# Kernel optimization log

Measured on AMD Instinct MI355X. Metric: run time of the kernel, lower is better.

Reference implementation:

```python
import jax, jax.numpy as jnp
import numpy as np

DIM = 1024
EXP = 4           # expansion_factor
NUM_EXPERTS = 4
BATCH, SEQ = 4, 4096


def setup_inputs() -> dict:
    key = jax.random.key(0)
    ks = jax.random.split(key, 6)
    x = jax.random.normal(ks[0], (BATCH, SEQ, DIM), dtype=jnp.float32)
    token_mask = jax.random.randint(ks[1], (BATCH, SEQ), 0, NUM_EXPERTS, dtype=jnp.int32)
    hid = DIM * EXP
    s1 = 1.0 / np.sqrt(DIM)
    s2 = 1.0 / np.sqrt(hid)
    # nn.Linear layout: weight [out_features, in_features]
    w1 = jax.random.uniform(ks[2], (hid, DIM), minval=-s1, maxval=s1, dtype=jnp.float32)
    b1 = jax.random.uniform(ks[3], (hid,), minval=-s1, maxval=s1, dtype=jnp.float32)
    w2 = jax.random.uniform(ks[4], (DIM, hid), minval=-s2, maxval=s2, dtype=jnp.float32)
    b2 = jax.random.uniform(ks[5], (DIM,), minval=-s2, maxval=s2, dtype=jnp.float32)
    return {"x": x, "w1": w1, "b1": b1, "w2": w2, "b2": b2, "token_mask": token_mask}


def _nested_ffn(x, w1, b1, w2, b2, token_mask):
    dim = x.shape[-1]            # in_features of proj1
    out_dim = w2.shape[0]        # out_features of proj2 (== dim)
    # Expert m uses the first D_m = width >> (E-1-m) features (matryoshka nesting).
    # Expand (proj1): truncating input features to D_m and doing a full GEMM is
    # exactly equivalent to zeroing features >= D_m, so we mask then do one GEMM.
    d_in = dim >> (NUM_EXPERTS - 1 - token_mask)             # [B,S]
    in_mask = jnp.arange(dim) < d_in[..., None]              # [B,S,dim]
    h = jnp.einsum('bsd,fd->bsf', jnp.where(in_mask, x, jnp.zeros((), x.dtype)), w1) + b1
    h = jax.nn.gelu(h, approximate=False)                    # torch nn.GELU() default = erf
    # Contract (proj2): expert m produces only the first D_m outputs (incl. bias),
    # padded with zeros -> compute full GEMM then mask outputs.
    d_out = out_dim >> (NUM_EXPERTS - 1 - token_mask)        # [B,S]
    out_mask = jnp.arange(out_dim) < d_out[..., None]        # [B,S,out_dim]
    y = jnp.einsum('bsf,df->bsd', h, w2) + b2
    return jnp.where(out_mask, y, jnp.zeros((), y.dtype))


def reference(x, w1, b1, w2, b2, token_mask):
    return _nested_ffn(x, w1, b1, w2, b2, token_mask)
```

## Files before the change

kernel.cpp:

```cpp
#include <hip/hip_runtime.h>
#include <hip/hip_bf16.h>


typedef __bf16 bf16x8 __attribute__((ext_vector_type(8)));
typedef float f32x4 __attribute__((ext_vector_type(4)));

#define M_TOK   16384
#define DIM     1024
#define HID     4096

#define META_TK    40
#define META_BLK   64
#define META_MAP   256
#define META_RT    2560

__device__ inline unsigned int pk_bf16(float a, float b) {
  unsigned int r;
  asm("v_cvt_pk_bf16_f32 %0, %1, %2" : "=v"(r) : "v"(a), "v"(b));
  return r;
}

__device__ inline float gelu_f(float v) {
  float v2 = v * v;
  float w = v * fmaf(0.10294324f, v2, 2.30220830f);
  float e = __builtin_amdgcn_exp2f(-w);
  return v * __builtin_amdgcn_rcpf(1.0f + e);
}

__device__ inline void async_copy16(const void* g, void* s) {
  __builtin_amdgcn_global_load_lds(
      (const __attribute__((address_space(1))) unsigned int*)g,
      (__attribute__((address_space(3))) unsigned int*)s,
      16, 0, 0);
}

template<int ROWS, int LDK>
__device__ inline void stage_tile(const unsigned short* __restrict__ g,
                                  int row0, int k0, char* lds) {
  const char* gbase = (const char*)g;
  int tid = threadIdx.x;
#pragma unroll
  for (int i = 0; i < ROWS / 32; ++i) {
    int q = i * 256 + tid;
    int r = q >> 3;
    int c = q & 7;
    int gc = c ^ (r & 7);
    const void* gp = gbase + ((size_t)(row0 + r) * LDK + (size_t)k0 + gc * 8) * 2;
    async_copy16(gp, lds + (size_t)q * 16);
  }
}

__global__ __launch_bounds__(1024) void sortw_kernel(
    const int* __restrict__ tm,
    const float* __restrict__ w1,
    const float* __restrict__ w2,
    int* __restrict__ meta,
    unsigned short* __restrict__ w1b,
    unsigned short* __restrict__ w2b) {
  int tid = threadIdx.x;
  if (blockIdx.x != 0) {
    size_t i = (size_t)(blockIdx.x - 1) * 4096 + tid * 4;
    const float* src;
    unsigned short* dst;
    if (i < (size_t)HID * DIM) { src = w1; dst = w1b; }
    else { src = w2 - (size_t)HID * DIM; dst = w2b - (size_t)HID * DIM; }
    float4 v = *(const float4*)(src + i);
    uint2 o;
    o.x = pk_bf16(v.x, v.y);
    o.y = pk_bf16(v.z, v.w);
    *(uint2*)(dst + i) = o;
    return;
  }

  __shared__ unsigned short rt[16384];
  __shared__ unsigned int w01[16], w23[16];
  __shared__ int sbase[4];
  __shared__ int cb[128];
  int lane = tid & 63, wv = tid >> 6;

  int c0 = 0, c1 = 0, c2 = 0, c3 = 0;
  unsigned int epack = 0;
  int4 tv[4];
#pragma unroll
  for (int j = 0; j < 4; ++j)
    tv[j] = *(const int4*)(tm + tid * 16 + j * 4);
#pragma unroll
  for (int j = 0; j < 4; ++j) {
    int e;
    e = tv[j].x; epack |= (unsigned)e << (2 * (4 * j + 0)); c0 += (e == 0); c1 += (e == 1); c2 += (e == 2); c3 += (e == 3);
    e = tv[j].y; epack |= (unsigned)e << (2 * (4 * j + 1)); c0 += (e == 0); c1 += (e == 1); c2 += (e == 2); c3 += (e == 3);
    e = tv[j].z; epack |= (unsigned)e << (2 * (4 * j + 2)); c0 += (e == 0); c1 += (e == 1); c2 += (e == 2); c3 += (e == 3);
    e = tv[j].w; epack |= (unsigned)e << (2 * (4 * j + 3)); c0 += (e == 0); c1 += (e == 1); c2 += (e == 2); c3 += (e == 3);
  }
  unsigned int p01 = (unsigned)c0 | ((unsigned)c1 << 16);
  unsigned int p23 = (unsigned)c2 | ((unsigned)c3 << 16);
  unsigned int i01 = p01, i23 = p23;
#pragma unroll
  for (int s = 1; s < 64; s <<= 1) {
    unsigned int t0 = __shfl_up(i01, s, 64);
    unsigned int t1 = __shfl_up(i23, s, 64);
    if (lane >= s) { i01 += t0; i23 += t1; }
  }
  if (lane == 63) { w01[wv] = i01; w23[wv] = i23; }
  unsigned int e01 = i01 - p01, e23 = i23 - p23;
  __syncthreads();
  if (tid < 16) {
    unsigned int a = w01[tid], b = w23[tid];
    unsigned int ia = a, ib = b;
#pragma unroll
    for (int s = 1; s < 16; s <<= 1) {
      unsigned int t0 = __shfl_up(ia, s, 64);
      unsigned int t1 = __shfl_up(ib, s, 64);
      if (tid >= s) { ia += t0; ib += t1; }
    }
    w01[tid] = ia - a;
    w23[tid] = ib - b;
    if (tid == 15) {
      int t0 = (int)(ia & 0xFFFF), t1 = (int)(ia >> 16), t2 = (int)(ib & 0xFFFF);
      sbase[0] = 0; sbase[1] = t0; sbase[2] = t0 + t1; sbase[3] = t0 + t1 + t2;
    }
  }
  __syncthreads();
  int off0 = sbase[0] + (int)((w01[wv] & 0xFFFF) + (e01 & 0xFFFF));
  int off1 = sbase[1] + (int)((w01[wv] >> 16) + (e01 >> 16));
  int off2 = sbase[2] + (int)((w23[wv] & 0xFFFF) + (e23 & 0xFFFF));
  int off3 = sbase[3] + (int)((w23[wv] >> 16) + (e23 >> 16));
#pragma unroll
  for (int j = 0; j < 16; ++j) {
    int e = (epack >> (2 * j)) & 3;
    int t = tid * 16 + j;
    int pos = (e == 0) ? off0++ : (e == 1) ? off1++ : (e == 2) ? off2++ : off3++;
    rt[pos] = (unsigned short)(t | (e << 14));
  }
  __syncthreads();

  if (tid < 128) {
    int last = tid * 128 + 127;
    int e = (last >= sbase[1]) + (last >= sbase[2]) + (last >= sbase[3]);
    cb[tid] = 1 << e;
    meta[META_BLK + tid] = 128 << e;
  }
  __syncthreads();
  if (tid < 8) {
    int k = tid;
    int* map = meta + META_MAP + k * 128;
    int Tk = 0;
    for (int j = 0; j < 16; ++j) Tk += cb[k + 8 * j];
    meta[META_TK + k] = Tk;
    int pos = 0, zpos = Tk;
    for (int j = 0; j < 16; ++j) {
      int s = k + 8 * j;
      int n = cb[s];
      for (int c = 0; c < n; ++c) map[pos++] = s * 8 + c;
      for (int c = n; c < 8; ++c) map[zpos++] = s * 8 + c;
    }
  }
  int* rowtok = meta + META_RT;
#pragma unroll
  for (int j = 0; j < 16; ++j)
    rowtok[j * 1024 + tid] = (int)rt[j * 1024 + tid];
}

__global__ void prepx_kernel(const float* __restrict__ x,
                             const int* __restrict__ meta,
                             unsigned short* __restrict__ xb) {
  int b = blockIdx.x;
  int tid = threadIdx.x;
  int mt = meta[META_RT + b];
  int t = mt & 0x3FFF;
  int din = 128 << (mt >> 14);
  int kb = meta[META_BLK + (b >> 7)];
  int d = tid * 4;
  if (d < kb) {
    uint2 o; o.x = 0; o.y = 0;
    if (d < din) {
      float4 v = *(const float4*)(x + (size_t)t * DIM + d);
      o.x = pk_bf16(v.x, v.y);
      o.y = pk_bf16(v.z, v.w);
    }
    *(uint2*)(xb + (size_t)b * DIM + d) = o;
  }
}

__global__ __launch_bounds__(256) void gemm1_kernel(
    const unsigned short* __restrict__ A,
    const unsigned short* __restrict__ B,
    const float* __restrict__ bias,
    const int* __restrict__ meta,
    unsigned short* __restrict__ H)
{
  constexpr int K = DIM, N = HID;
  __shared__ char smem[65536];
  int tid = threadIdx.x;
  int lane = tid & 63, quad = lane >> 4, l15 = lane & 15;
  int wave = tid >> 6, wm = wave & 1, wn = wave >> 1;
  int rowblk = 127 - (blockIdx.x >> 5);
  int row0 = rowblk * 128, col0 = (blockIdx.x & 31) * 128;
  int kmax = meta[META_BLK + rowblk];

  int chb = (quad ^ (l15 & 7)) << 4;

  f32x4 acc[4][4] = {};

  stage_tile<128, K>(A, row0, 0, smem);
  stage_tile<128, K>(B, col0, 0, smem + 16384);

  int nt = kmax >> 6;
  for (int t = 0; t < nt; ++t) {
    char* buf = smem + ((t & 1) << 15);
    if (t + 1 < nt) {
      char* nbuf = smem + (((t + 1) & 1) << 15);
      int kn = (t + 1) << 6;
      stage_tile<128, K>(A, row0, kn, nbuf);
      stage_tile<128, K>(B, col0, kn, nbuf + 16384);
      asm volatile("s_waitcnt vmcnt(8)" ::: "memory");
    } else {
      asm volatile("s_waitcnt vmcnt(0)" ::: "memory");
    }
    __builtin_amdgcn_s_barrier();
    char* As = buf;
    char* Bs = buf + 16384;
#pragma unroll
    for (int kk = 0; kk < 2; ++kk) {
      int xo = chb ^ (kk << 6);
      bf16x8 af[4], bg[4];
#pragma unroll
      for (int mt = 0; mt < 4; ++mt)
        af[mt] = *(const bf16x8*)(As + (wm * 64 + mt * 16 + l15) * 128 + xo);
#pragma unroll
      for (int nt2 = 0; nt2 < 4; ++nt2)
        bg[nt2] = *(const bf16x8*)(Bs + (wn * 64 + nt2 * 16 + l15) * 128 + xo);
#pragma unroll
      for (int mt = 0; mt < 4; ++mt)
#pragma unroll
        for (int nt2 = 0; nt2 < 4; ++nt2)
          acc[mt][nt2] = __builtin_amdgcn_mfma_f32_16x16x32_bf16(
              bg[nt2], af[mt], acc[mt][nt2], 0, 0, 0);
    }
    __builtin_amdgcn_s_barrier();
  }

  int t_base = row0 + wm * 64;
  int f_base = col0 + wn * 64;
#pragma unroll
  for (int nt2 = 0; nt2 < 4; ++nt2) {
    int f0 = f_base + nt2 * 16 + quad * 4;
    float4 bv = *(const float4*)(bias + f0);
#pragma unroll
    for (int mt = 0; mt < 4; ++mt) {
      int t = t_base + mt * 16 + l15;
      float v0 = gelu_f(acc[mt][nt2][0] + bv.x);
      float v1 = gelu_f(acc[mt][nt2][1] + bv.y);
      float v2 = gelu_f(acc[mt][nt2][2] + bv.z);
      float v3 = gelu_f(acc[mt][nt2][3] + bv.w);
      uint2 p;
      p.x = pk_bf16(v0, v1);
      p.y = pk_bf16(v2, v3);
      *(uint2*)(H + (size_t)t * N + f0) = p;
    }
  }
}

__global__ __launch_bounds__(256) void gemm2_kernel(
    const unsigned short* __restrict__ A,
    const unsigned short* __restrict__ B,
    const float* __restrict__ bias,
    const int* __restrict__ meta,
    float* __restrict__ out)
{
  constexpr int K = HID, N = DIM;
  int Bk = blockIdx.x & 7, ord = blockIdx.x >> 3;
  int Tk = meta[META_TK + Bk];
  int mp = meta[META_MAP + Bk * 128 + ord];
  int row0 = (mp >> 3) * 128, col0 = (mp & 7) * 128;
  const int* rowtok = meta + META_RT;
  int tid = threadIdx.x;

  if (ord >= Tk) {
    float4 z = make_float4(0.f, 0.f, 0.f, 0.f);
#pragma unroll
    for (int i = 0; i < 16; ++i) {
      int idx = i * 256 + tid;
      int r = idx >> 5;
      int col = (idx & 31) * 4;
      int t = rowtok[row0 + r] & 0x3FFF;
      *(float4*)(out + (size_t)t * N + col0 + col) = z;
    }
    return;
  }

  __shared__ char smem[65536];
  int lane = tid & 63, quad = lane >> 4, l15 = lane & 15;
  int wave = tid >> 6, wm = wave & 1, wn = wave >> 1;
  int chb = (quad ^ (l15 & 7)) << 4;

  f32x4 acc[4][4] = {};

  stage_tile<128, K>(A, row0, 0, smem);
  stage_tile<128, K>(B, col0, 0, smem + 16384);

  constexpr int NT = K >> 6;
  for (int t = 0; t < NT; ++t) {
    char* buf = smem + ((t & 1) << 15);
    if (t + 1 < NT) {
      char* nbuf = smem + (((t + 1) & 1) << 15);
      int kn = (t + 1) << 6;
      stage_tile<128, K>(A, row0, kn, nbuf);
      stage_tile<128, K>(B, col0, kn, nbuf + 16384);
      asm volatile("s_waitcnt vmcnt(8)" ::: "memory");
    } else {
      asm volatile("s_waitcnt vmcnt(0)" ::: "memory");
    }
    __builtin_amdgcn_s_barrier();
    char* As = buf;
    char* Bs = buf + 16384;
#pragma unroll
    for (int kk = 0; kk < 2; ++kk) {
      int xo = chb ^ (kk << 6);
      bf16x8 af[4], bg[4];
#pragma unroll
      for (int mt = 0; mt < 4; ++mt)
        af[mt] = *(const bf16x8*)(As + (wm * 64 + mt * 16 + l15) * 128 + xo);
#pragma unroll
      for (int nt2 = 0; nt2 < 4; ++nt2)
        bg[nt2] = *(const bf16x8*)(Bs + (wn * 64 + nt2 * 16 + l15) * 128 + xo);
#pragma unroll
      for (int mt = 0; mt < 4; ++mt)
#pragma unroll
        for (int nt2 = 0; nt2 < 4; ++nt2)
          acc[mt][nt2] = __builtin_amdgcn_mfma_f32_16x16x32_bf16(
              bg[nt2], af[mt], acc[mt][nt2], 0, 0, 0);
    }
    __builtin_amdgcn_s_barrier();
  }

  int p_base = row0 + wm * 64;
  int d_base = col0 + wn * 64;
  float4 bv[4];
#pragma unroll
  for (int nt2 = 0; nt2 < 4; ++nt2)
    bv[nt2] = *(const float4*)(bias + d_base + nt2 * 16 + quad * 4);
#pragma unroll
  for (int mt = 0; mt < 4; ++mt) {
    int m2 = rowtok[p_base + mt * 16 + l15];
    int t = m2 & 0x3FFF;
    int dout = 128 << (m2 >> 14);
#pragma unroll
    for (int nt2 = 0; nt2 < 4; ++nt2) {
      int d0 = d_base + nt2 * 16 + quad * 4;
      bool ok = d0 < dout;
      float4 o;
      o.x = ok ? acc[mt][nt2][0] + bv[nt2].x : 0.0f;
      o.y = ok ? acc[mt][nt2][1] + bv[nt2].y : 0.0f;
      o.z = ok ? acc[mt][nt2][2] + bv[nt2].z : 0.0f;
      o.w = ok ? acc[mt][nt2][3] + bv[nt2].w : 0.0f;
      *(float4*)(out + (size_t)t * N + d0) = o;
    }
  }
}

extern "C" void kernel_launch(void* const* d_in, const int* in_sizes, int n_in,
                              void* d_out, int out_size, void* d_ws, size_t ws_size,
                              hipStream_t stream) {
  const float* x  = (const float*)d_in[0];
  const float* w1 = (const float*)d_in[1];
  const float* b1 = (const float*)d_in[2];
  const float* w2 = (const float*)d_in[3];
  const float* b2 = (const float*)d_in[4];
  const int*   tm = (const int*)d_in[5];
  float* out = (float*)d_out;

  char* ws = (char*)d_ws;
  int* meta = (int*)ws;
  unsigned short* xb  = (unsigned short*)(ws + 131072);
  unsigned short* w1b = (unsigned short*)(ws + 33685504);
  unsigned short* w2b = (unsigned short*)(ws + 42074112);
  unsigned short* hb  = (unsigned short*)(ws + 50462720);

  sortw_kernel<<<2049, 1024, 0, stream>>>(tm, w1, w2, meta, w1b, w2b);
  prepx_kernel<<<M_TOK, 256, 0, stream>>>(x, meta, xb);
  gemm1_kernel<<<4096, 256, 0, stream>>>(xb, w1b, b1, meta, hb);
  gemm2_kernel<<<1024, 256, 0, stream>>>(hb, w2b, b2, meta, out);
}
```

Before: 302.6 us.

## Widen gemm2 tiles to 128x256 with 512-thread blocks and setprio

Changes gemm2 from 128x128 tiles with 256 threads to 128x256 tiles with 8 waves and 512 threads. It rebuilds the per-expert column-block map in the sort kernel for 4 column blocks per row block. It also raises wave priority around the MFMA section. The goal is to reuse each A tile across twice as many output columns, halving A traffic from the hidden buffer. The cost is 96KB of LDS per block, which limits occupancy, and coarser granularity for the masked column blocks.

Result: slower. 365.3 us (+20.7%).

```diff
diff --git a/kernel.cpp b/kernel.cpp
--- a/kernel.cpp
+++ b/kernel.cpp
@@ -34,14 +34,14 @@
       16, 0, 0);
 }
 
-template<int ROWS, int LDK>
+template<int ROWS, int LDK, int THREADS>
 __device__ inline void stage_tile(const unsigned short* __restrict__ g,
                                   int row0, int k0, char* lds) {
   const char* gbase = (const char*)g;
   int tid = threadIdx.x;
 #pragma unroll
-  for (int i = 0; i < ROWS / 32; ++i) {
-    int q = i * 256 + tid;
+  for (int i = 0; i < ROWS * 8 / THREADS; ++i) {
+    int q = i * THREADS + tid;
     int r = q >> 3;
     int c = q & 7;
     int gc = c ^ (r & 7);
@@ -137,13 +137,13 @@
   if (tid < 128) {
     int last = tid * 128 + 127;
     int e = (last >= sbase[1]) + (last >= sbase[2]) + (last >= sbase[3]);
-    cb[tid] = 1 << e;
     meta[META_BLK + tid] = 128 << e;
+    cb[tid] = (e < 2) ? 1 : (1 << (e - 1));
   }
   __syncthreads();
   if (tid < 8) {
     int k = tid;
-    int* map = meta + META_MAP + k * 128;
+    int* map = meta + META_MAP + k * 64;
     int Tk = 0;
     for (int j = 0; j < 16; ++j) Tk += cb[k + 8 * j];
     meta[META_TK + k] = Tk;
@@ -151,8 +151,8 @@
     for (int j = 0; j < 16; ++j) {
       int s = k + 8 * j;
       int n = cb[s];
-      for (int c = 0; c < n; ++c) map[pos++] = s * 8 + c;
-      for (int c = n; c < 8; ++c) map[zpos++] = s * 8 + c;
+      for (int c = 0; c < n; ++c) map[pos++] = s * 4 + c;
+      for (int c = n; c < 4; ++c) map[zpos++] = s * 4 + c;
     }
   }
   int* rowtok = meta + META_RT;
@@ -202,8 +202,8 @@
 
   f32x4 acc[4][4] = {};
 
-  stage_tile<128, K>(A, row0, 0, smem);
-  stage_tile<128, K>(B, col0, 0, smem + 16384);
+  stage_tile<128, K, 256>(A, row0, 0, smem);
+  stage_tile<128, K, 256>(B, col0, 0, smem + 16384);
 
   int nt = kmax >> 6;
   for (int t = 0; t < nt; ++t) {
@@ -211,8 +211,8 @@
     if (t + 1 < nt) {
       char* nbuf = smem + (((t + 1) & 1) << 15);
       int kn = (t + 1) << 6;
-      stage_tile<128, K>(A, row0, kn, nbuf);
-      stage_tile<128, K>(B, col0, kn, nbuf + 16384);
+      stage_tile<128, K, 256>(A, row0, kn, nbuf);
+      stage_tile<128, K, 256>(B, col0, kn, nbuf + 16384);
       asm volatile("s_waitcnt vmcnt(8)" ::: "memory");
     } else {
       asm volatile("s_waitcnt vmcnt(0)" ::: "memory");
@@ -261,7 +261,7 @@
   }
 }
 
-__global__ __launch_bounds__(256) void gemm2_kernel(
+__global__ __launch_bounds__(512, 2) void gemm2_kernel(
     const unsigned short* __restrict__ A,
     const unsigned short* __restrict__ B,
     const float* __restrict__ bias,
@@ -271,8 +271,8 @@
   constexpr int K = HID, N = DIM;
   int Bk = blockIdx.x & 7, ord = blockIdx.x >> 3;
   int Tk = meta[META_TK + Bk];
-  int mp = meta[META_MAP + Bk * 128 + ord];
-  int row0 = (mp >> 3) * 128, col0 = (mp & 7) * 128;
+  int mp = meta[META_MAP + Bk * 64 + ord];
+  int row0 = (mp >> 2) * 128, col0 = (mp & 3) * 256;
   const int* rowtok = meta + META_RT;
   int tid = threadIdx.x;
 
@@ -280,40 +280,42 @@
     float4 z = make_float4(0.f, 0.f, 0.f, 0.f);
 #pragma unroll
     for (int i = 0; i < 16; ++i) {
-      int idx = i * 256 + tid;
-      int r = idx >> 5;
-      int col = (idx & 31) * 4;
+      int idx = i * 512 + tid;
+      int r = idx >> 6;
+      int col = (idx & 63) * 4;
       int t = rowtok[row0 + r] & 0x3FFF;
       *(float4*)(out + (size_t)t * N + col0 + col) = z;
     }
     return;
   }
 
-  __shared__ char smem[65536];
+  __shared__ char smem[98304];
   int lane = tid & 63, quad = lane >> 4, l15 = lane & 15;
-  int wave = tid >> 6, wm = wave & 1, wn = wave >> 1;
+  int wave = tid >> 6;
+  int wm = wave >> 2, wn = wave & 3;
   int chb = (quad ^ (l15 & 7)) << 4;
 
   f32x4 acc[4][4] = {};
 
-  stage_tile<128, K>(A, row0, 0, smem);
-  stage_tile<128, K>(B, col0, 0, smem + 16384);
+  stage_tile<128, K, 512>(A, row0, 0, smem);
+  stage_tile<256, K, 512>(B, col0, 0, smem + 16384);
 
   constexpr int NT = K >> 6;
   for (int t = 0; t < NT; ++t) {
-    char* buf = smem + ((t & 1) << 15);
+    char* buf = smem + (t & 1) * 49152;
     if (t + 1 < NT) {
-      char* nbuf = smem + (((t + 1) & 1) << 15);
+      char* nbuf = smem + ((t + 1) & 1) * 49152;
       int kn = (t + 1) << 6;
-      stage_tile<128, K>(A, row0, kn, nbuf);
-      stage_tile<128, K>(B, col0, kn, nbuf + 16384);
-      asm volatile("s_waitcnt vmcnt(8)" ::: "memory");
+      stage_tile<128, K, 512>(A, row0, kn, nbuf);
+      stage_tile<256, K, 512>(B, col0, kn, nbuf + 16384);
+      asm volatile("s_waitcnt vmcnt(6)" ::: "memory");
     } else {
       asm volatile("s_waitcnt vmcnt(0)" ::: "memory");
     }
     __builtin_amdgcn_s_barrier();
     char* As = buf;
     char* Bs = buf + 16384;
+    __builtin_amdgcn_s_setprio(1);
 #pragma unroll
     for (int kk = 0; kk < 2; ++kk) {
       int xo = chb ^ (kk << 6);
@@ -322,15 +324,16 @@
       for (int mt = 0; mt < 4; ++mt)
         af[mt] = *(const bf16x8*)(As + (wm * 64 + mt * 16 + l15) * 128 + xo);
 #pragma unroll
-      for (int nt2 = 0; nt2 < 4; ++nt2)
-        bg[nt2] = *(const bf16x8*)(Bs + (wn * 64 + nt2 * 16 + l15) * 128 + xo);
+      for (int nf = 0; nf < 4; ++nf)
+        bg[nf] = *(const bf16x8*)(Bs + (wn * 64 + nf * 16 + l15) * 128 + xo);
 #pragma unroll
       for (int mt = 0; mt < 4; ++mt)
 #pragma unroll
-        for (int nt2 = 0; nt2 < 4; ++nt2)
-          acc[mt][nt2] = __builtin_amdgcn_mfma_f32_16x16x32_bf16(
-              bg[nt2], af[mt], acc[mt][nt2], 0, 0, 0);
-    }
+        for (int nf = 0; nf < 4; ++nf)
+          acc[mt][nf] = __builtin_amdgcn_mfma_f32_16x16x32_bf16(
+              bg[nf], af[mt], acc[mt][nf], 0, 0, 0);
+    }
+    __builtin_amdgcn_s_setprio(0);
     __builtin_amdgcn_s_barrier();
   }
 
@@ -338,22 +341,22 @@
   int d_base = col0 + wn * 64;
   float4 bv[4];
 #pragma unroll
-  for (int nt2 = 0; nt2 < 4; ++nt2)
-    bv[nt2] = *(const float4*)(bias + d_base + nt2 * 16 + quad * 4);
+  for (int nf = 0; nf < 4; ++nf)
+    bv[nf] = *(const float4*)(bias + d_base + nf * 16 + quad * 4);
 #pragma unroll
   for (int mt = 0; mt < 4; ++mt) {
     int m2 = rowtok[p_base + mt * 16 + l15];
     int t = m2 & 0x3FFF;
     int dout = 128 << (m2 >> 14);
 #pragma unroll
-    for (int nt2 = 0; nt2 < 4; ++nt2) {
-      int d0 = d_base + nt2 * 16 + quad * 4;
+    for (int nf = 0; nf < 4; ++nf) {
+      int d0 = d_base + nf * 16 + quad * 4;
       bool ok = d0 < dout;
       float4 o;
-      o.x = ok ? acc[mt][nt2][0] + bv[nt2].x : 0.0f;
-      o.y = ok ? acc[mt][nt2][1] + bv[nt2].y : 0.0f;
-      o.z = ok ? acc[mt][nt2][2] + bv[nt2].z : 0.0f;
-      o.w = ok ? acc[mt][nt2][3] + bv[nt2].w : 0.0f;
+      o.x = ok ? acc[mt][nf][0] + bv[nf].x : 0.0f;
+      o.y = ok ? acc[mt][nf][1] + bv[nf].y : 0.0f;
+      o.z = ok ? acc[mt][nf][2] + bv[nf].z : 0.0f;
+      o.w = ok ? acc[mt][nf][3] + bv[nf].w : 0.0f;
       *(float4*)(out + (size_t)t * N + d0) = o;
     }
   }
@@ -380,5 +383,5 @@
   sortw_kernel<<<2049, 1024, 0, stream>>>(tm, w1, w2, meta, w1b, w2b);
   prepx_kernel<<<M_TOK, 256, 0, stream>>>(x, meta, xb);
   gemm1_kernel<<<4096, 256, 0, stream>>>(xb, w1b, b1, meta, hb);
-  gemm2_kernel<<<1024, 256, 0, stream>>>(hb, w2b, b2, meta, out);
-}
+  gemm2_kernel<<<512, 512, 0, stream>>>(hb, w2b, b2, meta, out);
+}
```
